# Optimization experiments

Measured on AMD Instinct MI355X. Metric: run time of the kernel, lower is better.

The kernel has to match this reference:

```python
import jax, jax.numpy as jnp
import numpy as np

B, K, N = 8, 4, 131072
T = B * K * N  # upper bound on packed length
NEG_IDLE = -1e8   # logit value forced when slot is idle
NEG_FILL = -1000.0  # padded-output fill value for logits


def setup_inputs() -> dict:
    key = jax.random.key(0)
    k1, k2, k3, k4, k5, k6 = jax.random.split(key, 6)
    return {
        "rgb": jax.random.normal(k1, (T, 3), dtype=jnp.float32),
        "logits_surface": jax.random.normal(k2, (T, 1), dtype=jnp.float32),
        "logits_air": jax.random.normal(k3, (T, 1), dtype=jnp.float32),
        "mask_surface": jax.random.bernoulli(k4, 0.5, (B, K, N)),
        "mask_air": jax.random.bernoulli(k5, 0.5, (B, K, N)),
        "idle_states": jax.random.uniform(k6, (B, K), dtype=jnp.float32),
    }


def reference(rgb, logits_surface, logits_air, mask_surface, mask_air, idle_states):
    # Packed arrays are laid out in flattened (b, k, n) order: the packed index of a
    # masked element equals the count of True entries preceding it -> cumsum - 1.
    Bb, Kk, Nn = mask_surface.shape
    scale = (1.0 - idle_states)[:, :, None, None]          # [B,K,1,1]
    idle = idle_states[:, :, None, None]                   # [B,K,1,1]

    ms_flat = mask_surface.reshape(-1)
    idx_s = (jnp.cumsum(ms_flat.astype(jnp.int32)) - 1).reshape(Bb, Kk, Nn)
    ms = mask_surface[..., None]                           # [B,K,N,1]

    rgb_g = jnp.take(rgb, idx_s, axis=0)                   # [B,K,N,3]
    rgb_out = jnp.where(ms, rgb_g * scale, 0.0)

    ls_g = jnp.take(logits_surface, idx_s, axis=0)         # [B,K,N,1]
    logits_surface_out = jnp.where(ms, ls_g * scale + idle * NEG_IDLE, NEG_FILL)

    ma_flat = mask_air.reshape(-1)
    idx_a = (jnp.cumsum(ma_flat.astype(jnp.int32)) - 1).reshape(Bb, Kk, Nn)
    ma = mask_air[..., None]
    la_g = jnp.take(logits_air, idx_a, axis=0)             # [B,K,N,1]
    logits_air_out = jnp.where(ma, la_g * scale + idle * NEG_IDLE, NEG_FILL)

    return rgb_out, logits_surface_out, logits_air_out
```

## Files before the change

kernel.cpp:

```cpp
#include <hip/hip_runtime.h>
#include <stdint.h>

#define T_TOTAL  4194304
#define NEG_IDLE (-100000000.0f)
#define NEG_FILL (-1000.0f)

#define BLOCK   256
#define EPT     8
#define EPB     (BLOCK * EPT)
#define NBLOCKS (T_TOTAL / EPB)

#define SWZ(d) ((d) + ((d) >> 5))

typedef unsigned int u32x4 __attribute__((ext_vector_type(4)));
typedef float        f32x4 __attribute__((ext_vector_type(4)));

__device__ __forceinline__ unsigned decode8_i32(const u32x4 a, const u32x4 b) {
    return (a.x ? 1u : 0u) | (a.y ? 2u : 0u) | (a.z ? 4u : 0u) | (a.w ? 8u : 0u)
         | (b.x ? 16u : 0u) | (b.y ? 32u : 0u) | (b.z ? 64u : 0u) | (b.w ? 128u : 0u);
}

__device__ __forceinline__ f32x4 mk4(float a, float b, float c, float d) {
    f32x4 v; v.x = a; v.y = b; v.z = c; v.w = d; return v;
}

__global__ __launch_bounds__(BLOCK) void reduce_pack_kernel(
    const u32x4* __restrict__ ms,
    const u32x4* __restrict__ ma,
    unsigned long long* __restrict__ sums,
    unsigned short* __restrict__ packed)
{
    const int blk  = blockIdx.x;
    const int tid  = threadIdx.x;
    const int lane = tid & 63;
    const int wave = tid >> 6;
    const size_t e = (size_t)blk * EPB + (size_t)tid * EPT;

    const u32x4* ps = ms + (e >> 2);
    const u32x4* pa = ma + (e >> 2);
    const u32x4 s0 = __builtin_nontemporal_load(ps);
    const u32x4 s1 = __builtin_nontemporal_load(ps + 1);
    const u32x4 a0 = __builtin_nontemporal_load(pa);
    const u32x4 a1 = __builtin_nontemporal_load(pa + 1);
    const unsigned bits_s = decode8_i32(s0, s1);
    const unsigned bits_a = decode8_i32(a0, a1);
    packed[blk * BLOCK + tid] = (unsigned short)(bits_s | (bits_a << 8));

    unsigned long long v =
        ((unsigned long long)(unsigned)__popc(bits_a) << 32) | (unsigned)__popc(bits_s);
    #pragma unroll
    for (int d = 32; d; d >>= 1) v += __shfl_down(v, d, 64);

    __shared__ unsigned long long w[BLOCK / 64];
    if (lane == 0) w[wave] = v;
    __syncthreads();
    if (tid == 0) sums[blk] = w[0] + w[1] + w[2] + w[3];
}

__global__ __launch_bounds__(BLOCK) void scatter_kernel(
    const float* __restrict__ rgb,
    const float* __restrict__ ls,
    const float* __restrict__ la,
    const unsigned long long* __restrict__ sums,
    const unsigned short* __restrict__ packed,
    const float* __restrict__ idle_states,
    float* __restrict__ out)
{
    __shared__ float rgbb[6340];
    __shared__ float lsb[2120];
    __shared__ unsigned long long wtot[BLOCK / 64];
    __shared__ unsigned long long wpre[BLOCK / 64];

    const int blk  = blockIdx.x;
    const int tid  = threadIdx.x;
    const int lane = tid & 63;
    const int wave = tid >> 6;

    const unsigned p = packed[blk * BLOCK + tid];
    const unsigned bits_s = p & 0xffu;
    const unsigned bits_a = p >> 8;
    const int cnt_s = (int)(unsigned)(sums[blk] & 0xffffffffu);

    unsigned long long acc = 0;
    {
        const ulonglong2* s2 = (const ulonglong2*)sums;
        const int i0 = tid * 8;
        #pragma unroll
        for (int q = 0; q < 4; ++q) {
            const ulonglong2 v = s2[tid * 4 + q];
            const int i = i0 + 2 * q;
            acc += (i     < blk) ? v.x : 0ull;
            acc += (i + 1 < blk) ? v.y : 0ull;
        }
        #pragma unroll
        for (int d = 32; d; d >>= 1) acc += __shfl_down(acc, d, 64);
    }

    const unsigned long long pk =
        ((unsigned long long)(unsigned)__popc(bits_a) << 32) | (unsigned)__popc(bits_s);
    unsigned long long incl = pk;
    #pragma unroll
    for (int d = 1; d < 64; d <<= 1) {
        unsigned long long t = __shfl_up(incl, d, 64);
        if (lane >= d) incl += t;
    }
    unsigned long long excl = incl - pk;

    if (lane == 63) wtot[wave] = incl;
    if (lane == 0)  wpre[wave] = acc;
    __syncthreads();
    #pragma unroll
    for (int w = 0; w < BLOCK / 64; ++w)
        if (w < wave) excl += wtot[w];
    const unsigned long long pre = wpre[0] + wpre[1] + wpre[2] + wpre[3];
    const unsigned long long st  = pre + excl;

    const int start_s = (int)(unsigned)(pre & 0xffffffffu);
    const int idx_a0  = (int)(st >> 32);
    const int loc_s0  = (int)(unsigned)(st & 0xffffffffu) - start_s;

    int ls_[EPT], ia_[EPT];
    #pragma unroll
    for (int j = 0; j < EPT; ++j) {
        ls_[j] = loc_s0 + __popc(bits_s & ((1u << j) - 1u));
        ia_[j] = idx_a0 + __popc(bits_a & ((1u << j) - 1u));
    }

    float av[EPT];
    #pragma unroll
    for (int j = 0; j < EPT; ++j) av[j] = la[ia_[j]];

    const float* rgb_g = rgb + (size_t)start_s * 3;
    const float* ls_g  = ls + start_s;
    const int c3 = cnt_s * 3;
    float t24[24], t8[8];
    #pragma unroll
    for (int q = 0; q < 24; ++q) {
        const int d = tid + 256 * q;
        t24[q] = (d < c3) ? __builtin_nontemporal_load(rgb_g + d) : 0.0f;
    }
    #pragma unroll
    for (int q = 0; q < 8; ++q) {
        const int d = tid + 256 * q;
        t8[q] = (d < cnt_s) ? __builtin_nontemporal_load(ls_g + d) : 0.0f;
    }
    #pragma unroll
    for (int q = 0; q < 24; ++q) {
        const int d = tid + 256 * q;
        if (d < c3) rgbb[SWZ(d)] = t24[q];
    }
    #pragma unroll
    for (int q = 0; q < 8; ++q) {
        const int d = tid + 256 * q;
        if (d < cnt_s) lsb[SWZ(d)] = t8[q];
    }
    __syncthreads();

    float r[3 * EPT], sv[EPT];
    #pragma unroll
    for (int j = 0; j < EPT; ++j) {
        const int b = ls_[j] * 3;
        r[3 * j + 0] = rgbb[SWZ(b)];
        r[3 * j + 1] = rgbb[SWZ(b + 1)];
        r[3 * j + 2] = rgbb[SWZ(b + 2)];
        sv[j] = lsb[SWZ(ls_[j])];
    }
    __syncthreads();

    const float idle      = idle_states[blk >> 6];
    const float scale     = 1.0f - idle;
    const float idle_term = idle * NEG_IDLE;
    #pragma unroll
    for (int j = 0; j < EPT; ++j) {
        const bool bs = (bits_s >> j) & 1u;
        const bool ba = (bits_a >> j) & 1u;
        r[3 * j + 0] = bs ? r[3 * j + 0] * scale : 0.0f;
        r[3 * j + 1] = bs ? r[3 * j + 1] * scale : 0.0f;
        r[3 * j + 2] = bs ? r[3 * j + 2] * scale : 0.0f;
        sv[j] = bs ? (sv[j] * scale + idle_term) : NEG_FILL;
        av[j] = ba ? (av[j] * scale + idle_term) : NEG_FILL;
    }

    const size_t base = (size_t)blk * EPB + (size_t)tid * EPT;
    {
        f32x4* pls = (f32x4*)(out + (size_t)3 * T_TOTAL + base);
        __builtin_nontemporal_store(mk4(sv[0], sv[1], sv[2], sv[3]), pls);
        __builtin_nontemporal_store(mk4(sv[4], sv[5], sv[6], sv[7]), pls + 1);
        f32x4* pla = (f32x4*)(out + (size_t)4 * T_TOTAL + base);
        __builtin_nontemporal_store(mk4(av[0], av[1], av[2], av[3]), pla);
        __builtin_nontemporal_store(mk4(av[4], av[5], av[6], av[7]), pla + 1);
    }

    #pragma unroll
    for (int j = 0; j < 3 * EPT; ++j) {
        const int e = tid * 24 + j;
        rgbb[SWZ(e)] = r[j];
    }
    __syncthreads();
    float* out_rgb = out + (size_t)blk * (EPB * 3);
    #pragma unroll
    for (int i = 0; i < 6; ++i) {
        const int g = tid * 4 + 1024 * i;
        const f32x4 v = mk4(rgbb[SWZ(g)], rgbb[SWZ(g + 1)],
                            rgbb[SWZ(g + 2)], rgbb[SWZ(g + 3)]);
        __builtin_nontemporal_store(v, (f32x4*)(out_rgb + g));
    }
}

extern "C" void kernel_launch(void* const* d_in, const int* in_sizes, int n_in,
                              void* d_out, int out_size, void* d_ws, size_t ws_size,
                              hipStream_t stream) {
    const float* rgb  = (const float*)d_in[0];
    const float* ls   = (const float*)d_in[1];
    const float* la   = (const float*)d_in[2];
    const u32x4* ms   = (const u32x4*)d_in[3];
    const u32x4* ma   = (const u32x4*)d_in[4];
    const float* idle = (const float*)d_in[5];
    float* out = (float*)d_out;

    unsigned long long* sums   = (unsigned long long*)d_ws;
    unsigned short*     packed = (unsigned short*)((uint8_t*)d_ws + NBLOCKS * sizeof(unsigned long long));

    reduce_pack_kernel<<<NBLOCKS, BLOCK, 0, stream>>>(ms, ma, sums, packed);
    scatter_kernel<<<NBLOCKS, BLOCK, 0, stream>>>(rgb, ls, la, sums, packed,
                                                  idle, out);
}
```

Baseline: 173.0 us.

## Stage RGB via direct global-to-LDS loads and gather logits from global

Replaces the register-staged copy of the packed RGB segment into shared memory with 16-byte global_load_lds DMA transfers, aligned down to a 4-float boundary with a delta offset. The LDS staging buffer for surface logits is dropped; those values are now gathered straight from global memory. This targets register pressure and the VGPR round trip of the staging loop. In exchange the swizzle is removed, which may add LDS bank conflicts on the strided reads, and the gathered loads may read past the segment into the tail of the buffer.

```diff
diff --git a/kernel.cpp b/kernel.cpp
--- a/kernel.cpp
+++ b/kernel.cpp
@@ -22,6 +22,12 @@
 
 __device__ __forceinline__ f32x4 mk4(float a, float b, float c, float d) {
     f32x4 v; v.x = a; v.y = b; v.z = c; v.w = d; return v;
+}
+
+__device__ __forceinline__ void gl2lds16(const float* g, float* l) {
+    __builtin_amdgcn_global_load_lds(
+        (const __attribute__((address_space(1))) void*)g,
+        (__attribute__((address_space(3))) void*)l, 16, 0, 0);
 }
 
 __global__ __launch_bounds__(BLOCK) void reduce_pack_kernel(
@@ -67,7 +73,6 @@
     float* __restrict__ out)
 {
     __shared__ float rgbb[6340];
-    __shared__ float lsb[2120];
     __shared__ unsigned long long wtot[BLOCK / 64];
     __shared__ unsigned long long wpre[BLOCK / 64];
 
@@ -126,44 +131,33 @@
         ia_[j] = idx_a0 + __popc(bits_a & ((1u << j) - 1u));
     }
 
-    float av[EPT];
-    #pragma unroll
-    for (int j = 0; j < EPT; ++j) av[j] = la[ia_[j]];
-
-    const float* rgb_g = rgb + (size_t)start_s * 3;
-    const float* ls_g  = ls + start_s;
-    const int c3 = cnt_s * 3;
-    float t24[24], t8[8];
-    #pragma unroll
-    for (int q = 0; q < 24; ++q) {
-        const int d = tid + 256 * q;
-        t24[q] = (d < c3) ? __builtin_nontemporal_load(rgb_g + d) : 0.0f;
-    }
-    #pragma unroll
-    for (int q = 0; q < 8; ++q) {
-        const int d = tid + 256 * q;
-        t8[q] = (d < cnt_s) ? __builtin_nontemporal_load(ls_g + d) : 0.0f;
-    }
-    #pragma unroll
-    for (int q = 0; q < 24; ++q) {
-        const int d = tid + 256 * q;
-        if (d < c3) rgbb[SWZ(d)] = t24[q];
-    }
-    #pragma unroll
-    for (int q = 0; q < 8; ++q) {
-        const int d = tid + 256 * q;
-        if (d < cnt_s) lsb[SWZ(d)] = t8[q];
-    }
-    __syncthreads();
-
-    float r[3 * EPT], sv[EPT];
-    #pragma unroll
-    for (int j = 0; j < EPT; ++j) {
-        const int b = ls_[j] * 3;
-        r[3 * j + 0] = rgbb[SWZ(b)];
-        r[3 * j + 1] = rgbb[SWZ(b + 1)];
-        r[3 * j + 2] = rgbb[SWZ(b + 2)];
-        sv[j] = lsb[SWZ(ls_[j])];
+    float sv[EPT], av[EPT];
+    #pragma unroll
+    for (int j = 0; j < EPT; ++j) {
+        sv[j] = __builtin_nontemporal_load(ls + (start_s + ls_[j]));
+        av[j] = __builtin_nontemporal_load(la + ia_[j]);
+    }
+
+    const int start3  = start_s * 3;
+    const int start3a = start3 & ~3;
+    const int delta   = start3 - start3a;
+    const int c3p     = cnt_s * 3 + delta;
+    const float* gbase = rgb + start3a;
+    #pragma unroll
+    for (int q = 0; q < 6; ++q) {
+        const int off = (q * 4 + wave) * 256;
+        if (off < c3p)
+            gl2lds16(gbase + off + lane * 4, &rgbb[off]);
+    }
+    __syncthreads();
+
+    float r[3 * EPT];
+    #pragma unroll
+    for (int j = 0; j < EPT; ++j) {
+        const int b = 3 * ls_[j] + delta;
+        r[3 * j + 0] = rgbb[b];
+        r[3 * j + 1] = rgbb[b + 1];
+        r[3 * j + 2] = rgbb[b + 2];
     }
     __syncthreads();
 
```

Measured after the change: 178.9 us. +3.4%, slower.
